# Performance work log

Measured on AMD Instinct MI355X. Metric: run time of the kernel, lower is better.

## Reference

```python
import jax, jax.numpy as jnp
import numpy as np
from jax import lax

B, S, HDIM = 4, 2048, 1024
H, D, L = 16, 64, 128
NB = S // L
EPS = 1e-8


def setup_inputs() -> dict:
    key = jax.random.key(0)
    ks = jax.random.split(key, 16)
    std = 0.02
    inp = {
        'f_in': jax.random.normal(ks[0], (B, S, HDIM), jnp.float32),
        'i_in': jax.random.normal(ks[1], (B, S, HDIM), jnp.float32),
        'z_in': jax.random.normal(ks[2], (B, S, HDIM), jnp.float32),
        'o_in': jax.random.normal(ks[3], (B, S, HDIM), jnp.float32),
        'c0': jax.random.normal(ks[4], (B, H, D), jnp.float32),
        'h0': jax.random.normal(ks[5], (B, H, D), jnp.float32),
        # weights stored (in, out) so forward is x @ W + b
        'Wf': std * jax.random.normal(ks[6], (HDIM, H * D), jnp.float32),
        'bf': jnp.zeros((H * D,), jnp.float32),
        'Wi': std * jax.random.normal(ks[7], (HDIM, H * D), jnp.float32),
        'bi': jnp.zeros((H * D,), jnp.float32),
        'Wz': std * jax.random.normal(ks[8], (HDIM, H * D), jnp.float32),
        'bz': jnp.zeros((H * D,), jnp.float32),
        'Wo': std * jax.random.normal(ks[9], (HDIM, H * D), jnp.float32),
        'bo': jnp.zeros((H * D,), jnp.float32),
        'Wp': std * jax.random.normal(ks[10], (H * D, HDIM), jnp.float32),
        'bp': jnp.zeros((HDIM,), jnp.float32),
    }
    return inp


def _to_blocks(x):
    # (B,S,H*D) -> (NB, B, H, D, L), matching torch view+permute(1,0,3,4,2)
    return jnp.transpose(x.reshape(B, NB, L, H, D), (1, 0, 3, 4, 2))


def _qlstm(f_in, i_in, z_in, o_in, c0, Wf, bf, Wi, bi, Wz, bz, Wo, bo, Wp, bp):
    fx = _to_blocks(f_in @ Wf + bf)
    ix = _to_blocks(i_in @ Wi + bi)
    zx = _to_blocks(z_in @ Wz + bz)
    ox = _to_blocks(o_in @ Wo + bo)

    f = jax.nn.sigmoid(fx + 1.0)              # (NB,B,H,D,L)
    o = jax.nn.sigmoid(ox)
    update = jax.nn.sigmoid(ix) * jnp.tanh(zx)

    kk = jnp.arange(L)[:, None]
    ll = jnp.arange(L + 1)[None, :]
    ones_mask = ll >= kk + 1                   # (L, L+1): filled with 1.0
    zeros_mask = ll >= kk + 2                  # (L, L+1): zeroed out

    def block_step(c, blk):
        fb, ob, ub = blk                       # each (B,H,D,L)
        cf = jnp.concatenate([fb, jnp.ones(fb.shape[:-1] + (1,), fb.dtype)], axis=-1)  # (B,H,D,L+1)
        Fm = jnp.broadcast_to(cf[..., None, :], fb.shape[:-1] + (L, L + 1))
        Fm = jnp.where(ones_mask, 1.0, Fm)
        # reversed log-cumsum-exp along last axis (decay products)
        Fm = jnp.exp(jnp.flip(jnp.cumsum(jnp.flip(jnp.log(Fm + EPS), -1), -1), -1)) - EPS
        Fm = jnp.where(zeros_mask, 0.0, Fm)    # (B,H,D,L,L+1)
        u = jnp.concatenate([c[..., None], ub], axis=-1)   # (B,H,D,L+1)
        cs = jnp.einsum('bhdkl,bhdl->bhdk', Fm, u)          # (B,H,D,L)
        hs = ob * jnp.tanh(cs)
        return cs[..., -1], hs

    last_c, hs = lax.scan(block_step, c0, (f, o, update))   # hs: (NB,B,H,D,L)
    last_h = hs[-1, ..., -1]
    y = jnp.transpose(hs, (1, 0, 4, 2, 3)).reshape(B, S, H * D)
    y = y @ Wp + bp                            # (B,S,HDIM)
    return y, last_c, last_h


def reference(f_in, i_in, z_in, o_in, c0, h0, Wf, bf, Wi, bi, Wz, bz, Wo, bo, Wp, bp):
    y, last_c, last_h = _qlstm(f_in, i_in, z_in, o_in, c0,
                               Wf, bf, Wi, bi, Wz, bz, Wo, bo, Wp, bp)
    return y, last_c, last_h
```

## Files before the change

### kernel.cpp

```cpp
#include <hip/hip_runtime.h>
#include <hip/hip_bf16.h>
#include <stdint.h>

constexpr int GM = 8192;
constexpr int GK = 1024;
constexpr int GN = 1024;
constexpr size_t NACT = (size_t)GM * GN;
constexpr int CHUNK = 32;
constexpr int NCHUNK = 64;
constexpr int NCH = 4096;

#define DEVINL __device__ __forceinline__

typedef __attribute__((ext_vector_type(8))) short bf16x8;
typedef __attribute__((ext_vector_type(4))) float f32x4;

DEVINL float sigmoidf_(float x) { return 1.0f / (1.0f + __expf(-x)); }

DEVINL unsigned short f2bf(float x) {
  unsigned int u = __builtin_bit_cast(unsigned int, x);
  unsigned int rnd = 0x7fffu + ((u >> 16) & 1u);
  return (unsigned short)((u + rnd) >> 16);
}
DEVINL float bf2f(unsigned short u) {
  unsigned int x = ((unsigned int)u) << 16;
  return __builtin_bit_cast(float, x);
}

DEVINL void gload16(const void* g, void* l) {
  __builtin_amdgcn_global_load_lds(
      (const __attribute__((address_space(1))) unsigned int*)g,
      (__attribute__((address_space(3))) unsigned int*)l, 16, 0, 0);
}

__global__ void cvt_bf16_kernel(const float* __restrict__ src,
                                unsigned short* __restrict__ dst, int n4) {
  int i = blockIdx.x * blockDim.x + threadIdx.x;
  int stride = gridDim.x * blockDim.x;
  for (; i < n4; i += stride) {
    float4 v = ((const float4*)src)[i];
    ushort4 o;
    o.x = f2bf(v.x); o.y = f2bf(v.y); o.z = f2bf(v.z); o.w = f2bf(v.w);
    ((ushort4*)dst)[i] = o;
  }
}

__global__ void transpose_cvt_kernel(const float* __restrict__ W,
                                     unsigned short* __restrict__ Wt) {
  __shared__ float tile[32][33];
  int n0 = blockIdx.x * 32, k0 = blockIdx.y * 32;
  int tx = threadIdx.x & 31, ty = threadIdx.x >> 5;
#pragma unroll
  for (int i = 0; i < 32; i += 8)
    tile[ty + i][tx] = W[(size_t)(k0 + ty + i) * GN + n0 + tx];
  __syncthreads();
#pragma unroll
  for (int i = 0; i < 32; i += 8)
    Wt[(size_t)(n0 + ty + i) * GK + k0 + tx] = f2bf(tile[tx][ty + i]);
}

template <int MODE>
__global__ __launch_bounds__(256) void gemm128(
    const unsigned short* __restrict__ A1, const unsigned short* __restrict__ W1,
    const float* __restrict__ bias1,
    const unsigned short* __restrict__ A2, const unsigned short* __restrict__ W2,
    const float* __restrict__ bias2,
    unsigned short* __restrict__ outb, float* __restrict__ outf) {
  __shared__ __align__(16) unsigned short As[128 * 32];
  __shared__ __align__(16) unsigned short Bs[128 * 32];
  const int tid = threadIdx.x;
  const int wave = tid >> 6, lane = tid & 63;
  const int bm = blockIdx.x, bn = blockIdx.y;
  const int wm = (wave >> 1) * 64, wn = (wave & 1) * 64;
  const int lrow = lane & 15, lko = (lane >> 4) * 8;
  const int srow = tid >> 2, scol = (tid & 3) * 8;

  f32x4 acc1[4][4];
  f32x4 acc2[4][4];
#pragma unroll
  for (int m = 0; m < 4; ++m)
#pragma unroll
    for (int n = 0; n < 4; ++n) {
      acc1[m][n] = (f32x4){0.f, 0.f, 0.f, 0.f};
      acc2[m][n] = (f32x4){0.f, 0.f, 0.f, 0.f};
    }

  auto run = [&](const unsigned short* __restrict__ A,
                 const unsigned short* __restrict__ W, f32x4(&acc)[4][4]) {
    for (int k0 = 0; k0 < GK; k0 += 32) {
      __syncthreads();
      gload16(A + (size_t)(bm * 128 + srow) * GK + k0 + scol,
              (char*)As + wave * 1024);
      gload16(A + (size_t)(bm * 128 + 64 + srow) * GK + k0 + scol,
              (char*)As + 4096 + wave * 1024);
      gload16(W + (size_t)(bn * 128 + srow) * GK + k0 + scol,
              (char*)Bs + wave * 1024);
      gload16(W + (size_t)(bn * 128 + 64 + srow) * GK + k0 + scol,
              (char*)Bs + 4096 + wave * 1024);
      __syncthreads();

      bf16x8 af[4], bfr[4];
#pragma unroll
      for (int m = 0; m < 4; ++m)
        af[m] = *(const bf16x8*)&As[(wm + m * 16 + lrow) * 32 + lko];
#pragma unroll
      for (int n = 0; n < 4; ++n)
        bfr[n] = *(const bf16x8*)&Bs[(wn + n * 16 + lrow) * 32 + lko];
#pragma unroll
      for (int m = 0; m < 4; ++m)
#pragma unroll
        for (int n = 0; n < 4; ++n)
          acc[m][n] = __builtin_amdgcn_mfma_f32_16x16x32_bf16(af[m], bfr[n],
                                                              acc[m][n], 0, 0, 0);
    }
  };

  run(A1, W1, acc1);
  if constexpr (MODE == 2) run(A2, W2, acc2);

  float b1v[4], b2v[4];
#pragma unroll
  for (int n = 0; n < 4; ++n) {
    int gc = bn * 128 + wn + n * 16 + lrow;
    b1v[n] = bias1[gc];
    if constexpr (MODE == 2) b2v[n] = bias2[gc];
    else b2v[n] = 0.f;
  }

#pragma unroll
  for (int m = 0; m < 4; ++m) {
#pragma unroll
    for (int n = 0; n < 4; ++n) {
      int gc = bn * 128 + wn + n * 16 + lrow;
#pragma unroll
      for (int j = 0; j < 4; ++j) {
        int gr = bm * 128 + wm + m * 16 + (lane >> 4) * 4 + j;
        float v = acc1[m][n][j] + b1v[n];
        size_t oidx = (size_t)gr * GN + gc;
        if constexpr (MODE == 0) {
          outb[oidx] = f2bf(sigmoidf_(v + 1.0f));
        } else if constexpr (MODE == 1) {
          outb[oidx] = f2bf(sigmoidf_(v));
        } else if constexpr (MODE == 2) {
          float v2 = acc2[m][n][j] + b2v[n];
          outb[oidx] = f2bf(sigmoidf_(v) * tanhf(v2));
        } else {
          outf[oidx] = v;
        }
      }
    }
  }
}

__global__ void scan_phaseA_kernel(const unsigned short* __restrict__ F,
                                   const unsigned short* __restrict__ U,
                                   float* __restrict__ Pt, float* __restrict__ Ct) {
  int tid = blockIdx.x * blockDim.x + threadIdx.x;
  int ch = tid & (NCH - 1), chunk = tid >> 12;
  int b = ch >> 10, n = ch & 1023;
  size_t base = ((size_t)(b * 2048 + chunk * CHUNK)) * 1024 + n;
  float c = 0.f, P = 1.f;
#pragma unroll 8
  for (int t = 0; t < CHUNK; ++t) {
    size_t idx = base + (size_t)t * 1024;
    float f = bf2f(F[idx]);
    float u = bf2f(U[idx]);
    c = __builtin_fmaf(f, c, u);
    P *= f;
  }
  Pt[tid] = P;
  Ct[tid] = c;
}

__global__ void scan_combine_kernel(const float* __restrict__ Pt,
                                    const float* __restrict__ Ct,
                                    const float* __restrict__ c0,
                                    float* __restrict__ Cin,
                                    float* __restrict__ last_c) {
  int ch = blockIdx.x * blockDim.x + threadIdx.x;
  float c = c0[ch];
#pragma unroll
  for (int j = 0; j < NCHUNK; ++j) {
    Cin[j * NCH + ch] = c;
    c = __builtin_fmaf(Pt[j * NCH + ch], c, Ct[j * NCH + ch]);
  }
  last_c[ch] = c;
}

__global__ void scan_phaseC_kernel(const unsigned short* __restrict__ F,
                                   const unsigned short* __restrict__ U,
                                   const unsigned short* __restrict__ O,
                                   const float* __restrict__ Cin,
                                   unsigned short* __restrict__ Hb,
                                   float* __restrict__ last_h) {
  int tid = blockIdx.x * blockDim.x + threadIdx.x;
  int ch = tid & (NCH - 1), chunk = tid >> 12;
  int b = ch >> 10, n = ch & 1023;
  size_t base = ((size_t)(b * 2048 + chunk * CHUNK)) * 1024 + n;
  float c = Cin[tid];
  float h = 0.f;
#pragma unroll 8
  for (int t = 0; t < CHUNK; ++t) {
    size_t idx = base + (size_t)t * 1024;
    float f = bf2f(F[idx]);
    float u = bf2f(U[idx]);
    float o = bf2f(O[idx]);
    c = __builtin_fmaf(f, c, u);
    h = o * tanhf(c);
    Hb[idx] = f2bf(h);
  }
  if (chunk == NCHUNK - 1) last_h[ch] = h;
}

extern "C" void kernel_launch(void* const* d_in, const int* in_sizes, int n_in,
                              void* d_out, int out_size, void* d_ws, size_t ws_size,
                              hipStream_t stream) {
  const float* f_in = (const float*)d_in[0];
  const float* i_in = (const float*)d_in[1];
  const float* z_in = (const float*)d_in[2];
  const float* o_in = (const float*)d_in[3];
  const float* c0 = (const float*)d_in[4];
  const float* Wf = (const float*)d_in[6];
  const float* bf_ = (const float*)d_in[7];
  const float* Wi = (const float*)d_in[8];
  const float* bi = (const float*)d_in[9];
  const float* Wz = (const float*)d_in[10];
  const float* bz = (const float*)d_in[11];
  const float* Wo = (const float*)d_in[12];
  const float* bo = (const float*)d_in[13];
  const float* Wp = (const float*)d_in[14];
  const float* bp = (const float*)d_in[15];

  float* y = (float*)d_out;
  float* last_c = y + NACT;
  float* last_h = last_c + NCH;

  char* w = (char*)d_ws;
  const size_t ABYTES = NACT * 2;
  const size_t WBYTES = (size_t)GK * GN * 2;
  unsigned short* Af = (unsigned short*)(w + 0 * ABYTES);
  unsigned short* Ai = (unsigned short*)(w + 1 * ABYTES);
  unsigned short* Az = (unsigned short*)(w + 2 * ABYTES);
  unsigned short* Ao = (unsigned short*)(w + 3 * ABYTES);
  char* wt = w + 4 * ABYTES;
  unsigned short* Wtf = (unsigned short*)(wt + 0 * WBYTES);
  unsigned short* Wti = (unsigned short*)(wt + 1 * WBYTES);
  unsigned short* Wtz = (unsigned short*)(wt + 2 * WBYTES);
  unsigned short* Wto = (unsigned short*)(wt + 3 * WBYTES);
  unsigned short* Wtp = (unsigned short*)(wt + 4 * WBYTES);
  char* gp = wt + 5 * WBYTES;
  unsigned short* F = (unsigned short*)(gp + 0 * ABYTES);
  unsigned short* U = (unsigned short*)(gp + 1 * ABYTES);
  unsigned short* O = (unsigned short*)(gp + 2 * ABYTES);
  unsigned short* Hb = (unsigned short*)(gp + 3 * ABYTES);
  char* sp = gp + 4 * ABYTES;
  const size_t SBYTES = (size_t)NCH * NCHUNK * 4;
  float* Pt = (float*)(sp + 0 * SBYTES);
  float* Ct = (float*)(sp + 1 * SBYTES);
  float* Cin = (float*)(sp + 2 * SBYTES);

  const int n4 = (int)(NACT / 4);
  cvt_bf16_kernel<<<2048, 256, 0, stream>>>(f_in, Af, n4);
  cvt_bf16_kernel<<<2048, 256, 0, stream>>>(i_in, Ai, n4);
  cvt_bf16_kernel<<<2048, 256, 0, stream>>>(z_in, Az, n4);
  cvt_bf16_kernel<<<2048, 256, 0, stream>>>(o_in, Ao, n4);

  dim3 tg(32, 32);
  transpose_cvt_kernel<<<tg, 256, 0, stream>>>(Wf, Wtf);
  transpose_cvt_kernel<<<tg, 256, 0, stream>>>(Wi, Wti);
  transpose_cvt_kernel<<<tg, 256, 0, stream>>>(Wz, Wtz);
  transpose_cvt_kernel<<<tg, 256, 0, stream>>>(Wo, Wto);
  transpose_cvt_kernel<<<tg, 256, 0, stream>>>(Wp, Wtp);

  dim3 gg(GM / 128, GN / 128);
  gemm128<0><<<gg, 256, 0, stream>>>(Af, Wtf, bf_, nullptr, nullptr, nullptr, F, nullptr);
  gemm128<1><<<gg, 256, 0, stream>>>(Ao, Wto, bo, nullptr, nullptr, nullptr, O, nullptr);
  gemm128<2><<<gg, 256, 0, stream>>>(Ai, Wti, bi, Az, Wtz, bz, U, nullptr);

  scan_phaseA_kernel<<<(NCH * NCHUNK) / 256, 256, 0, stream>>>(F, U, Pt, Ct);
  scan_combine_kernel<<<NCH / 256, 256, 0, stream>>>(Pt, Ct, c0, Cin, last_c);
  scan_phaseC_kernel<<<(NCH * NCHUNK) / 256, 256, 0, stream>>>(F, U, O, Cin, Hb, last_h);

  gemm128<3><<<gg, 256, 0, stream>>>(Hb, Wtp, bp, nullptr, nullptr, nullptr, nullptr, y);
}
```

Before: 238.7 us.

## Fuse fp32-to-bf16 activation conversion into gate GEMM loads and batch launches

Removes the four separate activation conversion kernels. The gate GEMMs now read the fp32 inputs directly, convert them to bf16 in registers and store them into LDS. The f and o gate GEMMs are merged into one launch using blockIdx.z, and the five weight transposes are merged into one launch. This saves writing and re-reading 64MB of bf16 activations plus several launch overheads. In exchange, A-tile loads become synchronous register loads instead of async global_load_lds, and each GEMM block re-reads the fp32 A tile once per N tile (8x), which raises GEMM read traffic and may expose latency.

```diff
diff --git a/kernel.cpp b/kernel.cpp
--- a/kernel.cpp
+++ b/kernel.cpp
@@ -13,6 +13,7 @@
 #define DEVINL __device__ __forceinline__
 
 typedef __attribute__((ext_vector_type(8))) short bf16x8;
+typedef __attribute__((ext_vector_type(8))) unsigned short u16x8;
 typedef __attribute__((ext_vector_type(4))) float f32x4;
 
 DEVINL float sigmoidf_(float x) { return 1.0f / (1.0f + __expf(-x)); }
@@ -33,20 +34,14 @@
       (__attribute__((address_space(3))) unsigned int*)l, 16, 0, 0);
 }
 
-__global__ void cvt_bf16_kernel(const float* __restrict__ src,
-                                unsigned short* __restrict__ dst, int n4) {
-  int i = blockIdx.x * blockDim.x + threadIdx.x;
-  int stride = gridDim.x * blockDim.x;
-  for (; i < n4; i += stride) {
-    float4 v = ((const float4*)src)[i];
-    ushort4 o;
-    o.x = f2bf(v.x); o.y = f2bf(v.y); o.z = f2bf(v.z); o.w = f2bf(v.w);
-    ((ushort4*)dst)[i] = o;
-  }
-}
-
-__global__ void transpose_cvt_kernel(const float* __restrict__ W,
-                                     unsigned short* __restrict__ Wt) {
+struct TPtrs {
+  const float* src[5];
+  unsigned short* dst[5];
+};
+
+__global__ void transpose_cvt_all(TPtrs p) {
+  const float* __restrict__ W = p.src[blockIdx.z];
+  unsigned short* __restrict__ Wt = p.dst[blockIdx.z];
   __shared__ float tile[32][33];
   int n0 = blockIdx.x * 32, k0 = blockIdx.y * 32;
   int tx = threadIdx.x & 31, ty = threadIdx.x >> 5;
@@ -59,24 +54,118 @@
     Wt[(size_t)(n0 + ty + i) * GK + k0 + tx] = f2bf(tile[tx][ty + i]);
 }
 
-template <int MODE>
-__global__ __launch_bounds__(256) void gemm128(
-    const unsigned short* __restrict__ A1, const unsigned short* __restrict__ W1,
-    const float* __restrict__ bias1,
-    const unsigned short* __restrict__ A2, const unsigned short* __restrict__ W2,
-    const float* __restrict__ bias2,
-    unsigned short* __restrict__ outb, float* __restrict__ outf) {
+struct GemmCtx {
+  int wave, lane, bm, bn, wm, wn, lrow, lko, srow, scol8;
+};
+
+DEVINL GemmCtx make_ctx() {
+  GemmCtx c;
+  int tid = threadIdx.x;
+  c.wave = tid >> 6;
+  c.lane = tid & 63;
+  c.bm = blockIdx.x;
+  c.bn = blockIdx.y;
+  c.wm = (c.wave >> 1) * 64;
+  c.wn = (c.wave & 1) * 64;
+  c.lrow = c.lane & 15;
+  c.lko = (c.lane >> 4) * 8;
+  c.srow = tid >> 2;
+  c.scol8 = (tid & 3) * 8;
+  return c;
+}
+
+DEVINL void gemm_kloop_f32A(const GemmCtx& c, const float* __restrict__ A,
+                            const unsigned short* __restrict__ W,
+                            unsigned short* As, unsigned short* Bs,
+                            f32x4 (&acc)[4][4]) {
+  const int wave = c.wave;
+  for (int k0 = 0; k0 < GK; k0 += 32) {
+    __syncthreads();
+    const float* a0p = A + (size_t)(c.bm * 128 + c.srow) * GK + k0 + c.scol8;
+    const float* a1p = a0p + (size_t)64 * GK;
+    float4 v0 = *(const float4*)(a0p);
+    float4 v1 = *(const float4*)(a0p + 4);
+    float4 v2 = *(const float4*)(a1p);
+    float4 v3 = *(const float4*)(a1p + 4);
+    gload16(W + (size_t)(c.bn * 128 + c.srow) * GK + k0 + c.scol8,
+            (char*)Bs + wave * 1024);
+    gload16(W + (size_t)(c.bn * 128 + 64 + c.srow) * GK + k0 + c.scol8,
+            (char*)Bs + 4096 + wave * 1024);
+    u16x8 p0, p1;
+    p0[0] = f2bf(v0.x); p0[1] = f2bf(v0.y); p0[2] = f2bf(v0.z); p0[3] = f2bf(v0.w);
+    p0[4] = f2bf(v1.x); p0[5] = f2bf(v1.y); p0[6] = f2bf(v1.z); p0[7] = f2bf(v1.w);
+    p1[0] = f2bf(v2.x); p1[1] = f2bf(v2.y); p1[2] = f2bf(v2.z); p1[3] = f2bf(v2.w);
+    p1[4] = f2bf(v3.x); p1[5] = f2bf(v3.y); p1[6] = f2bf(v3.z); p1[7] = f2bf(v3.w);
+    *(u16x8*)&As[c.srow * 32 + c.scol8] = p0;
+    *(u16x8*)&As[(c.srow + 64) * 32 + c.scol8] = p1;
+    __syncthreads();
+
+    bf16x8 af[4], bfr[4];
+#pragma unroll
+    for (int m = 0; m < 4; ++m)
+      af[m] = *(const bf16x8*)&As[(c.wm + m * 16 + c.lrow) * 32 + c.lko];
+#pragma unroll
+    for (int n = 0; n < 4; ++n)
+      bfr[n] = *(const bf16x8*)&Bs[(c.wn + n * 16 + c.lrow) * 32 + c.lko];
+#pragma unroll
+    for (int m = 0; m < 4; ++m)
+#pragma unroll
+      for (int n = 0; n < 4; ++n)
+        acc[m][n] = __builtin_amdgcn_mfma_f32_16x16x32_bf16(af[m], bfr[n],
+                                                            acc[m][n], 0, 0, 0);
+  }
+}
+
+__global__ __launch_bounds__(256) void gemm_gates_fo(
+    const float* __restrict__ Aa, const unsigned short* __restrict__ Wa,
+    const float* __restrict__ ba, unsigned short* __restrict__ outa,
+    const float* __restrict__ Ab, const unsigned short* __restrict__ Wb,
+    const float* __restrict__ bb, unsigned short* __restrict__ outb) {
   __shared__ __align__(16) unsigned short As[128 * 32];
   __shared__ __align__(16) unsigned short Bs[128 * 32];
-  const int tid = threadIdx.x;
-  const int wave = tid >> 6, lane = tid & 63;
-  const int bm = blockIdx.x, bn = blockIdx.y;
-  const int wm = (wave >> 1) * 64, wn = (wave & 1) * 64;
-  const int lrow = lane & 15, lko = (lane >> 4) * 8;
-  const int srow = tid >> 2, scol = (tid & 3) * 8;
-
-  f32x4 acc1[4][4];
-  f32x4 acc2[4][4];
+  const bool second = blockIdx.z != 0;
+  const float* A = second ? Ab : Aa;
+  const unsigned short* W = second ? Wb : Wa;
+  const float* bias = second ? bb : ba;
+  unsigned short* out = second ? outb : outa;
+  const float addc = second ? 0.0f : 1.0f;
+
+  GemmCtx c = make_ctx();
+  f32x4 acc[4][4];
+#pragma unroll
+  for (int m = 0; m < 4; ++m)
+#pragma unroll
+    for (int n = 0; n < 4; ++n) acc[m][n] = (f32x4){0.f, 0.f, 0.f, 0.f};
+
+  gemm_kloop_f32A(c, A, W, As, Bs, acc);
+
+  float bv[4];
+#pragma unroll
+  for (int n = 0; n < 4; ++n) bv[n] = bias[c.bn * 128 + c.wn + n * 16 + c.lrow];
+
+#pragma unroll
+  for (int m = 0; m < 4; ++m)
+#pragma unroll
+    for (int n = 0; n < 4; ++n) {
+      int gc = c.bn * 128 + c.wn + n * 16 + c.lrow;
+#pragma unroll
+      for (int j = 0; j < 4; ++j) {
+        int gr = c.bm * 128 + c.wm + m * 16 + (c.lane >> 4) * 4 + j;
+        float v = acc[m][n][j] + bv[n] + addc;
+        out[(size_t)gr * GN + gc] = f2bf(sigmoidf_(v));
+      }
+    }
+}
+
+__global__ __launch_bounds__(256) void gemm_gate_u(
+    const float* __restrict__ Ai, const unsigned short* __restrict__ Wi,
+    const float* __restrict__ bi,
+    const float* __restrict__ Az, const unsigned short* __restrict__ Wz,
+    const float* __restrict__ bz, unsigned short* __restrict__ out) {
+  __shared__ __align__(16) unsigned short As[128 * 32];
+  __shared__ __align__(16) unsigned short Bs[128 * 32];
+  GemmCtx c = make_ctx();
+  f32x4 acc1[4][4], acc2[4][4];
 #pragma unroll
   for (int m = 0; m < 4; ++m)
 #pragma unroll
@@ -85,71 +174,87 @@
       acc2[m][n] = (f32x4){0.f, 0.f, 0.f, 0.f};
     }
 
-  auto run = [&](const unsigned short* __restrict__ A,
-                 const unsigned short* __restrict__ W, f32x4(&acc)[4][4]) {
-    for (int k0 = 0; k0 < GK; k0 += 32) {
-      __syncthreads();
-      gload16(A + (size_t)(bm * 128 + srow) * GK + k0 + scol,
-              (char*)As + wave * 1024);
-      gload16(A + (size_t)(bm * 128 + 64 + srow) * GK + k0 + scol,
-              (char*)As + 4096 + wave * 1024);
-      gload16(W + (size_t)(bn * 128 + srow) * GK + k0 + scol,
-              (char*)Bs + wave * 1024);
-      gload16(W + (size_t)(bn * 128 + 64 + srow) * GK + k0 + scol,
-              (char*)Bs + 4096 + wave * 1024);
-      __syncthreads();
-
-      bf16x8 af[4], bfr[4];
-#pragma unroll
-      for (int m = 0; m < 4; ++m)
-        af[m] = *(const bf16x8*)&As[(wm + m * 16 + lrow) * 32 + lko];
-#pragma unroll
-      for (int n = 0; n < 4; ++n)
-        bfr[n] = *(const bf16x8*)&Bs[(wn + n * 16 + lrow) * 32 + lko];
-#pragma unroll
-      for (int m = 0; m < 4; ++m)
-#pragma unroll
-        for (int n = 0; n < 4; ++n)
-          acc[m][n] = __builtin_amdgcn_mfma_f32_16x16x32_bf16(af[m], bfr[n],
-                                                              acc[m][n], 0, 0, 0);
-    }
-  };
-
-  run(A1, W1, acc1);
-  if constexpr (MODE == 2) run(A2, W2, acc2);
+  gemm_kloop_f32A(c, Ai, Wi, As, Bs, acc1);
+  gemm_kloop_f32A(c, Az, Wz, As, Bs, acc2);
 
   float b1v[4], b2v[4];
 #pragma unroll
   for (int n = 0; n < 4; ++n) {
-    int gc = bn * 128 + wn + n * 16 + lrow;
-    b1v[n] = bias1[gc];
-    if constexpr (MODE == 2) b2v[n] = bias2[gc];
-    else b2v[n] = 0.f;
-  }
-
-#pragma unroll
-  for (int m = 0; m < 4; ++m) {
+    int gc = c.bn * 128 + c.wn + n * 16 + c.lrow;
+    b1v[n] = bi[gc];
+    b2v[n] = bz[gc];
+  }
+
+#pragma unroll
+  for (int m = 0; m < 4; ++m)
 #pragma unroll
     for (int n = 0; n < 4; ++n) {
-      int gc = bn * 128 + wn + n * 16 + lrow;
+      int gc = c.bn * 128 + c.wn + n * 16 + c.lrow;
 #pragma unroll
       for (int j = 0; j < 4; ++j) {
-        int gr = bm * 128 + wm + m * 16 + (lane >> 4) * 4 + j;
-        float v = acc1[m][n][j] + b1v[n];
-        size_t oidx = (size_t)gr * GN + gc;
-        if constexpr (MODE == 0) {
-          outb[oidx] = f2bf(sigmoidf_(v + 1.0f));
-        } else if constexpr (MODE == 1) {
-          outb[oidx] = f2bf(sigmoidf_(v));
-        } else if constexpr (MODE == 2) {
-          float v2 = acc2[m][n][j] + b2v[n];
-          outb[oidx] = f2bf(sigmoidf_(v) * tanhf(v2));
-        } else {
-          outf[oidx] = v;
-        }
+        int gr = c.bm * 128 + c.wm + m * 16 + (c.lane >> 4) * 4 + j;
+        float vi = acc1[m][n][j] + b1v[n];
+        float vz = acc2[m][n][j] + b2v[n];
+        out[(size_t)gr * GN + gc] = f2bf(sigmoidf_(vi) * tanhf(vz));
       }
     }
-  }
+}
+
+__global__ __launch_bounds__(256) void gemm_proj(
+    const unsigned short* __restrict__ A, const unsigned short* __restrict__ W,
+    const float* __restrict__ bias, float* __restrict__ out) {
+  __shared__ __align__(16) unsigned short As[128 * 32];
+  __shared__ __align__(16) unsigned short Bs[128 * 32];
+  GemmCtx c = make_ctx();
+  const int wave = c.wave;
+  f32x4 acc[4][4];
+#pragma unroll
+  for (int m = 0; m < 4; ++m)
+#pragma unroll
+    for (int n = 0; n < 4; ++n) acc[m][n] = (f32x4){0.f, 0.f, 0.f, 0.f};
+
+  for (int k0 = 0; k0 < GK; k0 += 32) {
+    __syncthreads();
+    gload16(A + (size_t)(c.bm * 128 + c.srow) * GK + k0 + c.scol8,
+            (char*)As + wave * 1024);
+    gload16(A + (size_t)(c.bm * 128 + 64 + c.srow) * GK + k0 + c.scol8,
+            (char*)As + 4096 + wave * 1024);
+    gload16(W + (size_t)(c.bn * 128 + c.srow) * GK + k0 + c.scol8,
+            (char*)Bs + wave * 1024);
+    gload16(W + (size_t)(c.bn * 128 + 64 + c.srow) * GK + k0 + c.scol8,
+            (char*)Bs + 4096 + wave * 1024);
+    __syncthreads();
+
+    bf16x8 af[4], bfr[4];
+#pragma unroll
+    for (int m = 0; m < 4; ++m)
+      af[m] = *(const bf16x8*)&As[(c.wm + m * 16 + c.lrow) * 32 + c.lko];
+#pragma unroll
+    for (int n = 0; n < 4; ++n)
+      bfr[n] = *(const bf16x8*)&Bs[(c.wn + n * 16 + c.lrow) * 32 + c.lko];
+#pragma unroll
+    for (int m = 0; m < 4; ++m)
+#pragma unroll
+      for (int n = 0; n < 4; ++n)
+        acc[m][n] = __builtin_amdgcn_mfma_f32_16x16x32_bf16(af[m], bfr[n],
+                                                            acc[m][n], 0, 0, 0);
+  }
+
+  float bv[4];
+#pragma unroll
+  for (int n = 0; n < 4; ++n) bv[n] = bias[c.bn * 128 + c.wn + n * 16 + c.lrow];
+
+#pragma unroll
+  for (int m = 0; m < 4; ++m)
+#pragma unroll
+    for (int n = 0; n < 4; ++n) {
+      int gc = c.bn * 128 + c.wn + n * 16 + c.lrow;
+#pragma unroll
+      for (int j = 0; j < 4; ++j) {
+        int gr = c.bm * 128 + c.wm + m * 16 + (c.lane >> 4) * 4 + j;
+        out[(size_t)gr * GN + gc] = acc[m][n][j] + bv[n];
+      }
+    }
 }
 
 __global__ void scan_phaseA_kernel(const unsigned short* __restrict__ F,
@@ -236,19 +341,14 @@
   float* last_h = last_c + NCH;
 
   char* w = (char*)d_ws;
+  const size_t WBYTES = (size_t)GK * GN * 2;
+  unsigned short* Wtf = (unsigned short*)(w + 0 * WBYTES);
+  unsigned short* Wti = (unsigned short*)(w + 1 * WBYTES);
+  unsigned short* Wtz = (unsigned short*)(w + 2 * WBYTES);
+  unsigned short* Wto = (unsigned short*)(w + 3 * WBYTES);
+  unsigned short* Wtp = (unsigned short*)(w + 4 * WBYTES);
+  char* gp = w + 5 * WBYTES;
   const size_t ABYTES = NACT * 2;
-  const size_t WBYTES = (size_t)GK * GN * 2;
-  unsigned short* Af = (unsigned short*)(w + 0 * ABYTES);
-  unsigned short* Ai = (unsigned short*)(w + 1 * ABYTES);
-  unsigned short* Az = (unsigned short*)(w + 2 * ABYTES);
-  unsigned short* Ao = (unsigned short*)(w + 3 * ABYTES);
-  char* wt = w + 4 * ABYTES;
-  unsigned short* Wtf = (unsigned short*)(wt + 0 * WBYTES);
-  unsigned short* Wti = (unsigned short*)(wt + 1 * WBYTES);
-  unsigned short* Wtz = (unsigned short*)(wt + 2 * WBYTES);
-  unsigned short* Wto = (unsigned short*)(wt + 3 * WBYTES);
-  unsigned short* Wtp = (unsigned short*)(wt + 4 * WBYTES);
-  char* gp = wt + 5 * WBYTES;
   unsigned short* F = (unsigned short*)(gp + 0 * ABYTES);
   unsigned short* U = (unsigned short*)(gp + 1 * ABYTES);
   unsigned short* O = (unsigned short*)(gp + 2 * ABYTES);
@@ -259,27 +359,19 @@
   float* Ct = (float*)(sp + 1 * SBYTES);
   float* Cin = (float*)(sp + 2 * SBYTES);
 
-  const int n4 = (int)(NACT / 4);
-  cvt_bf16_kernel<<<2048, 256, 0, stream>>>(f_in, Af, n4);
-  cvt_bf16_kernel<<<2048, 256, 0, stream>>>(i_in, Ai, n4);
-  cvt_bf16_kernel<<<2048, 256, 0, stream>>>(z_in, Az, n4);
-  cvt_bf16_kernel<<<2048, 256, 0, stream>>>(o_in, Ao, n4);
-
-  dim3 tg(32, 32);
-  transpose_cvt_kernel<<<tg, 256, 0, stream>>>(Wf, Wtf);
-  transpose_cvt_kernel<<<tg, 256, 0, stream>>>(Wi, Wti);
-  transpose_cvt_kernel<<<tg, 256, 0, stream>>>(Wz, Wtz);
-  transpose_cvt_kernel<<<tg, 256, 0, stream>>>(Wo, Wto);
-  transpose_cvt_kernel<<<tg, 256, 0, stream>>>(Wp, Wtp);
-
-  dim3 gg(GM / 128, GN / 128);
-  gemm128<0><<<gg, 256, 0, stream>>>(Af, Wtf, bf_, nullptr, nullptr, nullptr, F, nullptr);
-  gemm128<1><<<gg, 256, 0, stream>>>(Ao, Wto, bo, nullptr, nullptr, nullptr, O, nullptr);
-  gemm128<2><<<gg, 256, 0, stream>>>(Ai, Wti, bi, Az, Wtz, bz, U, nullptr);
+  TPtrs tp;
+  tp.src[0] = Wf; tp.src[1] = Wi; tp.src[2] = Wz; tp.src[3] = Wo; tp.src[4] = Wp;
+  tp.dst[0] = Wtf; tp.dst[1] = Wti; tp.dst[2] = Wtz; tp.dst[3] = Wto; tp.dst[4] = Wtp;
+  transpose_cvt_all<<<dim3(32, 32, 5), 256, 0, stream>>>(tp);
+
+  gemm_gates_fo<<<dim3(GM / 128, GN / 128, 2), 256, 0, stream>>>(
+      f_in, Wtf, bf_, F, o_in, Wto, bo, O);
+  gemm_gate_u<<<dim3(GM / 128, GN / 128), 256, 0, stream>>>(
+      i_in, Wti, bi, z_in, Wtz, bz, U);
 
   scan_phaseA_kernel<<<(NCH * NCHUNK) / 256, 256, 0, stream>>>(F, U, Pt, Ct);
   scan_combine_kernel<<<NCH / 256, 256, 0, stream>>>(Pt, Ct, c0, Cin, last_c);
   scan_phaseC_kernel<<<(NCH * NCHUNK) / 256, 256, 0, stream>>>(F, U, O, Cin, Hb, last_h);
 
-  gemm128<3><<<gg, 256, 0, stream>>>(Hb, Wtp, bp, nullptr, nullptr, nullptr, nullptr, y);
-}
+  gemm_proj<<<dim3(GM / 128, GN / 128), 256, 0, stream>>>(Hb, Wtp, bp, y);
+}
```

After: 251.3 us. 1.05x slower.
